# Performance work log

Hardware: AMD Instinct MI355X
Metric: run time of the kernel (lower is better)

Reference implementation:

```python
import jax, jax.numpy as jnp
import numpy as np

BETA = 0.05
KNN = 6
UL_ALPHA = 0.05
UL_BETA = 1.0


def setup_inputs() -> dict:
    key = jax.random.key(0)
    k1, k2, k3 = jax.random.split(key, 3)
    B, D, N = 256, 2048, 16384
    inputs = jax.random.normal(k1, (B, D), dtype=jnp.float32)
    em = jax.random.normal(k2, (N, D), dtype=jnp.float32)
    # exemplar memory rows are kept unit-norm by the update rule
    em = em / jnp.linalg.norm(em, axis=1, keepdims=True)
    targets = jax.random.randint(k3, (B,), 0, N, dtype=jnp.int64)
    return {"inputs": inputs, "em": em, "targets": targets, "epoch": 10}


def smooth_hot(logits, targets, em, k):
    # Vectorized k-reciprocal neighbor search (replaces the per-sample Python loop).
    m, n = logits.shape
    # index_sorted[:, :k] == top-k class indices per sample
    _, topk_idx = jax.lax.top_k(logits, k)            # [m, k]
    neigh = em[topk_idx]                               # [m, k, d]
    sims = jnp.einsum('mkd,nd->mkn', neigh, em)        # [m, k, n]
    _, neigh_topk = jax.lax.top_k(sims, k)             # [m, k, k]
    # neighbor j of sample i is reciprocal if anchor (top-1 of i) is in its top-k
    anchor = topk_idx[:, :1, None]                     # [m, 1, 1]
    recip = (neigh_topk == anchor).any(axis=-1)        # [m, k]
    weights = jnp.where(recip, 3.0 / k, 0.0).astype(logits.dtype)
    rows = jnp.arange(m)[:, None]
    onehot = jnp.zeros_like(logits).at[rows, topk_idx].set(weights)
    onehot = onehot.at[jnp.arange(m), targets].set(1.0)
    return onehot


def reference(inputs, em, targets, epoch):
    # ExemplarMemory.forward: similarity logits against the memory bank
    logits = (inputs @ em.T) / BETA                    # [B, N]
    # epoch >= 5 and knn > 0 branch (epoch=10)
    onehot = jax.lax.stop_gradient(
        smooth_hot(jax.lax.stop_gradient(logits), targets, em, KNN))
    logp = jax.nn.log_softmax(logits, axis=1)
    beta_loss = (-(onehot * logp).sum(axis=1)).mean()
    t_re = jnp.where(onehot == 0.0, jnp.float32(1e-4), onehot)
    alpha_loss = (-(jax.nn.softmax(logits, axis=1) * jnp.log(t_re)).sum(axis=1)).mean()
    return (UL_ALPHA * alpha_loss, UL_BETA * beta_loss)
```

## Files before the change

### kernel.cpp

```cpp
#include <hip/hip_runtime.h>
#include <math.h>

#define DIMK 2048
#define NEMB 16384
#define NB 256
#define NR2 1536
#define INV_BETA 20.0f
#define NEG_INF (-3.0e38f)

typedef short short8 __attribute__((ext_vector_type(8)));
typedef float f32x4 __attribute__((ext_vector_type(4)));

__device__ __forceinline__ unsigned short f2bf(float f) {
  unsigned u = __float_as_uint(f);
  u += 0x7fffu + ((u >> 16) & 1u);
  return (unsigned short)(u >> 16);
}

__device__ __forceinline__ void ins6i(float x, int xi, float v[6], int vi[6]) {
  if (x > v[5] || (x == v[5] && xi < vi[5])) {
    v[5] = x; vi[5] = xi;
#pragma unroll
    for (int j = 5; j > 0; j--) {
      if (v[j] > v[j - 1] || (v[j] == v[j - 1] && vi[j] < vi[j - 1])) {
        float tv = v[j]; v[j] = v[j - 1]; v[j - 1] = tv;
        int ti = vi[j]; vi[j] = vi[j - 1]; vi[j - 1] = ti;
      }
    }
  }
}

__global__ __launch_bounds__(256) void cvt_kernel(const float* __restrict__ src,
                                                  unsigned short* __restrict__ dst, int n4) {
  int i = blockIdx.x * 256 + threadIdx.x;
  if (i < n4) {
    float4 f = ((const float4*)src)[i];
    ushort4 o;
    o.x = f2bf(f.x); o.y = f2bf(f.y); o.z = f2bf(f.z); o.w = f2bf(f.w);
    ((ushort4*)dst)[i] = o;
  }
}

template <int MODE>
__global__ __launch_bounds__(256, 3) void gemm_rs(
    const unsigned short* __restrict__ Abase, const unsigned short* __restrict__ Bbase,
    const int* __restrict__ nidx, float* __restrict__ outP,
    const float* __restrict__ saIn, int* __restrict__ cntOut,
    const int* __restrict__ surv, const int* __restrict__ nsurvp) {
  constexpr int MTILE = (MODE == 0) ? 64 : 128;
  constexpr int MI = 4;
  constexpr int NI = (MODE == 0) ? 2 : 4;
  constexpr int NSUB_A = MTILE / 16;
  constexpr int NSUB = NSUB_A + 8;
  constexpr int NA = NSUB / 4;
  constexpr int NKC = (MODE == 1 || MODE == 2) ? 16 : 64;
  constexpr int OSTRIDE = (MODE == 0) ? 16384 : ((MODE == 1) ? 2048 : 14336);
  constexpr size_t PLANE =
      (MODE == 1) ? (size_t)1280 * 2048 : ((MODE == 2) ? (size_t)256 * 14336 : 0);

  __shared__ unsigned short st[2][NSUB * 512];
  __shared__ int rowIdxSh[128];
  __shared__ float saSh[128];
  __shared__ int cntSh[128];
  __shared__ int outRowSh[128];
  int t = threadIdx.x;
  int lane = t & 63, wave = t >> 6;
  int quad = lane >> 4, l16 = lane & 15;
  int wr = (MODE == 0) ? 0 : (wave >> 1);
  int wc = (MODE == 0) ? wave : (wave & 1);
  int bn = blockIdx.x, bm = blockIdx.y, kz = blockIdx.z;
  int nvalid = 128;

  if constexpr (MODE == 1) {
    if (t < 128) {
      int slot = bm * 128 + t;
      int g = (slot / 5) * 6 + (slot % 5) + 1;
      rowIdxSh[t] = nidx[g];
    }
    __syncthreads();
  }
  if constexpr (MODE == 2) {
    int ns = nsurvp[0];
    int nsCap = (ns < 256) ? ns : 256;
    if (bm * 128 >= nsCap) return;
    if (t < 128) {
      int idx = bm * 128 + t;
      rowIdxSh[t] = nidx[surv[(idx < nsCap) ? idx : 0]];
    }
    __syncthreads();
  }
  if constexpr (MODE == 3) {
    int ns = nsurvp[0];
    if (256 + bm * 128 >= ns) return;
    nvalid = ns - 256 - bm * 128;
    if (nvalid > 128) nvalid = 128;
    if (t < 128) {
      int idx = 256 + bm * 128 + ((t < nvalid) ? t : 0);
      int r = surv[idx];
      rowIdxSh[t] = nidx[r];
      saSh[t] = saIn[r];
      cntSh[t] = 0;
      outRowSh[t] = r;
    }
    __syncthreads();
  }

  int colbase = (MODE >= 2) ? ((bn + 16) * 128) : (bn * 128);
  int kbase = (MODE == 1 || MODE == 2) ? kz * (NKC * 32) : 0;

  const unsigned short* agp[NA];
  int soff[NA];
  {
    int seg = lane >> 4;
#pragma unroll
    for (int a = 0; a < NA; a++) {
      int s = wave + a * 4;
      size_t grow;
      const unsigned short* basep;
      if (s < NSUB_A) {
        int r = s * 16 + l16;
        grow = (MODE == 0) ? (size_t)(bm * MTILE + r) : (size_t)rowIdxSh[r];
        basep = Abase;
      } else {
        grow = (size_t)(colbase + (s - NSUB_A) * 16 + l16);
        basep = Bbase;
      }
      agp[a] = basep + grow * DIMK + kbase + seg * 8;
      soff[a] = s * 512;
    }
  }

  f32x4 acc[MI][NI];
#pragma unroll
  for (int mi = 0; mi < MI; mi++)
#pragma unroll
    for (int ni = 0; ni < NI; ni++) acc[mi][ni] = (f32x4)0.0f;

  int lo = lane * 8;

  short8 rA[NA], rB2[NA];
  auto LOADT = [&](short8* R, int kk) {
#pragma unroll
    for (int a = 0; a < NA; a++) R[a] = *(const short8*)(agp[a] + kk * 32);
  };
  auto WRITET = [&](const short8* R, int b) {
#pragma unroll
    for (int a = 0; a < NA; a++) *(short8*)&st[b][soff[a] + lo] = R[a];
  };
  auto COMPUTE = [&](int b) {
    const unsigned short* hb = &st[b][0];
    short8 af[MI], bfv[NI];
#pragma unroll
    for (int mi = 0; mi < MI; mi++)
      af[mi] = *(const short8*)&hb[(wr * MI + mi) * 512 + lo];
#pragma unroll
    for (int ni = 0; ni < NI; ni++)
      bfv[ni] = *(const short8*)&hb[(NSUB_A + wc * NI + ni) * 512 + lo];
#pragma unroll
    for (int mi = 0; mi < MI; mi++)
#pragma unroll
      for (int ni = 0; ni < NI; ni++)
        acc[mi][ni] =
            __builtin_amdgcn_mfma_f32_16x16x32_bf16(af[mi], bfv[ni], acc[mi][ni], 0, 0, 0);
  };

  LOADT(rA, 0);
  LOADT(rB2, 1);
  WRITET(rA, 0);
  __syncthreads();
  for (int k = 0; k < NKC; k += 2) {
    if (k + 2 < NKC) LOADT(rA, k + 2);
    COMPUTE(0);
    WRITET(rB2, 1);
    __syncthreads();
    if (k + 3 < NKC) LOADT(rB2, k + 3);
    COMPUTE(1);
    if (k + 2 < NKC) WRITET(rA, 0);
    __syncthreads();
  }

  if constexpr (MODE == 0) {
#pragma unroll
    for (int mi = 0; mi < MI; mi++) {
      int row = bm * MTILE + mi * 16 + quad * 4;
#pragma unroll
      for (int ni = 0; ni < NI; ni++) {
        int col = bn * 128 + wave * 32 + ni * 16 + l16;
#pragma unroll
        for (int rr = 0; rr < 4; rr++)
          outP[(size_t)(row + rr) * OSTRIDE + col] = acc[mi][ni][rr] * INV_BETA;
      }
    }
  } else if constexpr (MODE == 1 || MODE == 2) {
    float* op = outP + (size_t)kz * PLANE;
#pragma unroll
    for (int mi = 0; mi < MI; mi++) {
#pragma unroll
      for (int ni = 0; ni < NI; ni++) {
        int col = bn * 128 + wc * 64 + ni * 16 + l16;
#pragma unroll
        for (int rr = 0; rr < 4; rr++) {
          int row = bm * 128 + wr * 64 + mi * 16 + quad * 4 + rr;
          op[(size_t)row * OSTRIDE + col] = acc[mi][ni][rr];
        }
      }
    }
  } else {
#pragma unroll
    for (int mi = 0; mi < MI; mi++) {
#pragma unroll
      for (int rr = 0; rr < 4; rr++) {
        int rloc = wr * 64 + mi * 16 + quad * 4 + rr;
        float s = saSh[rloc];
        int c = 0;
#pragma unroll
        for (int ni = 0; ni < NI; ni++) c += (acc[mi][ni][rr] > s) ? 1 : 0;
        c += __shfl_xor(c, 1, 64);
        c += __shfl_xor(c, 2, 64);
        c += __shfl_xor(c, 4, 64);
        c += __shfl_xor(c, 8, 64);
        if (l16 == 0) atomicAdd(&cntSh[rloc], c);
      }
    }
    __syncthreads();
    if (t < nvalid) atomicAdd(&cntOut[outRowSh[t]], cntSh[t]);
  }
}

__global__ __launch_bounds__(256) void countA_kernel(const float* __restrict__ simsA,
                                                     const float* __restrict__ sa,
                                                     int* __restrict__ cnt) {
  int t = threadIdx.x, lane = t & 63;
  constexpr size_t PL = (size_t)1280 * 2048;
  for (int it = blockIdx.x; it < 1280 * 8; it += 256) {
    int slot = it >> 3, cx = it & 7;
    int g = (slot / 5) * 6 + (slot % 5) + 1;
    size_t o = (size_t)slot * 2048 + cx * 256 + t;
    float s = simsA[o] + simsA[o + PL] + simsA[o + 2 * PL] + simsA[o + 3 * PL];
    int c = (s > sa[g]) ? 1 : 0;
#pragma unroll
    for (int off = 32; off > 0; off >>= 1) c += __shfl_down(c, off, 64);
    if (lane == 0 && c > 0) atomicAdd(&cnt[g], c);
  }
}

__global__ __launch_bounds__(256) void countB_kernel(const float* __restrict__ simsB,
                                                     const float* __restrict__ sa,
                                                     const int* __restrict__ surv,
                                                     const int* __restrict__ nsurvp,
                                                     int* __restrict__ cnt) {
  int t = threadIdx.x, lane = t & 63;
  int ns = nsurvp[0];
  int nsCap = (ns < 256) ? ns : 256;
  constexpr size_t PL = (size_t)256 * 14336;
  int total = nsCap * 56;
  for (int it = blockIdx.x; it < total; it += 448) {
    int sv = it / 56, cx = it % 56;
    size_t o = (size_t)sv * 14336 + cx * 256 + t;
    float s = simsB[o] + simsB[o + PL] + simsB[o + 2 * PL] + simsB[o + 3 * PL];
    int w = surv[sv];
    int c = (s > sa[w]) ? 1 : 0;
#pragma unroll
    for (int off = 32; off > 0; off >>= 1) c += __shfl_down(c, off, 64);
    if (lane == 0 && c > 0) atomicAdd(&cnt[w], c);
  }
}

__global__ __launch_bounds__(256) void compact_kernel(const int* __restrict__ cnt,
                                                      int* __restrict__ surv,
                                                      int* __restrict__ nsurv) {
  __shared__ int ctr;
  if (threadIdx.x == 0) ctr = 0;
  __syncthreads();
  for (int i = threadIdx.x; i < NR2; i += 256) {
    if ((i % 6) != 0 && cnt[i] < 6) {
      int p = atomicAdd(&ctr, 1);
      surv[p] = i;
    }
  }
  __syncthreads();
  if (threadIdx.x == 0) nsurv[0] = ctr;
}

__global__ __launch_bounds__(1024) void rowstats_kernel(
    const float* __restrict__ logits, float* __restrict__ topv,
    int* __restrict__ topi, float* __restrict__ lse) {
  int m = blockIdx.x, t = threadIdx.x;
  const float4* row4 = (const float4*)(logits + (size_t)m * NEMB);
  float v6[6]; int i6[6];
#pragma unroll
  for (int j = 0; j < 6; j++) { v6[j] = NEG_INF; i6[j] = 0x7fffffff; }
  float vals[16];
#pragma unroll
  for (int j = 0; j < 4; j++) {
    float4 f = row4[t + j * 1024];
    vals[j * 4 + 0] = f.x; vals[j * 4 + 1] = f.y;
    vals[j * 4 + 2] = f.z; vals[j * 4 + 3] = f.w;
  }
  float mx = vals[0];
#pragma unroll
  for (int r = 1; r < 16; r++) mx = fmaxf(mx, vals[r]);
  float sme = 0.f;
#pragma unroll
  for (int r = 0; r < 16; r++) sme += expf(vals[r] - mx);
#pragma unroll
  for (int j = 0; j < 4; j++) {
    int base = (t + j * 1024) * 4;
#pragma unroll
    for (int b = 0; b < 4; b++) ins6i(vals[j * 4 + b], base + b, v6, i6);
  }
  __shared__ float sv[1024 * 6]; __shared__ int si[1024 * 6];
  __shared__ float smx[1024], ssm[1024];
#pragma unroll
  for (int j = 0; j < 6; j++) { sv[t * 6 + j] = v6[j]; si[t * 6 + j] = i6[j]; }
  smx[t] = mx; ssm[t] = sme;
  __syncthreads();
  for (int s = 512; s > 0; s >>= 1) {
    if (t < s) {
      float mo = smx[t + s], lo2 = ssm[t + s];
      float mn = fmaxf(smx[t], mo);
      ssm[t] = ssm[t] * expf(smx[t] - mn) + lo2 * expf(mo - mn);
      smx[t] = mn;
#pragma unroll
      for (int j = 0; j < 6; j++) ins6i(sv[(t + s) * 6 + j], si[(t + s) * 6 + j], v6, i6);
#pragma unroll
      for (int j = 0; j < 6; j++) { sv[t * 6 + j] = v6[j]; si[t * 6 + j] = i6[j]; }
    }
    __syncthreads();
  }
  if (t == 0) {
    lse[m] = smx[0] + logf(ssm[0]);
#pragma unroll
    for (int j = 0; j < 6; j++) { topv[m * 6 + j] = v6[j]; topi[m * 6 + j] = i6[j]; }
  }
}

__global__ __launch_bounds__(256) void sa_kernel(const float* __restrict__ em,
                                                 const int* __restrict__ topi,
                                                 float* __restrict__ sa,
                                                 int* __restrict__ cnt) {
  int gid = blockIdx.x * 256 + threadIdx.x;
  int w = gid >> 6, lane = gid & 63;
  if (w >= NR2) return;
  if (lane == 1) cnt[w] = 0;
  int m = w / 6;
  int i = topi[w], a = topi[m * 6];
  const float* ei = em + (size_t)i * DIMK;
  const float* ea = em + (size_t)a * DIMK;
  float s = 0.f;
  for (int d = lane; d < DIMK; d += 64) s += ei[d] * ea[d];
#pragma unroll
  for (int off = 32; off > 0; off >>= 1) s += __shfl_down(s, off, 64);
  if (lane == 0) sa[w] = s;
}

__global__ __launch_bounds__(256) void final_kernel(
    const float* __restrict__ logits, const float* __restrict__ topv,
    const int* __restrict__ topi, const float* __restrict__ lse_arr,
    const int* __restrict__ cnt, const int* __restrict__ targets,
    float* __restrict__ out) {
  int m = threadIdx.x;
  float lse = lse_arr[m];
  int tgt = targets[m];
  float tl = logits[(size_t)m * NEMB + tgt];
  float beta = 0.f, Ps = 0.f, nbp = 0.f;
  bool tin = false;
#pragma unroll
  for (int k = 0; k < 6; k++) {
    int idx = topi[m * 6 + k]; float v = topv[m * 6 + k];
    float p = expf(v - lse);
    if (idx == tgt) { tin = true; beta += (lse - v); Ps += p; }
    else if (cnt[m * 6 + k] < 6) { beta += 0.5f * (lse - v); Ps += p; nbp += p; }
  }
  if (!tin) { beta += (lse - tl); Ps += expf(tl - lse); }
  float alpha = 9.2103404f * (1.f - Ps) + 0.6931472f * nbp;
  __shared__ float sA[256], sB2[256];
  sA[m] = alpha; sB2[m] = beta;
  __syncthreads();
  for (int s = 128; s > 0; s >>= 1) {
    if (m < s) { sA[m] += sA[m + s]; sB2[m] += sB2[m + s]; }
    __syncthreads();
  }
  if (m == 0) { out[0] = 0.05f * sA[0] / 256.f; out[1] = sB2[0] / 256.f; }
}

extern "C" void kernel_launch(void* const* d_in, const int* in_sizes, int n_in,
                              void* d_out, int out_size, void* d_ws, size_t ws_size,
                              hipStream_t stream) {
  const float* x = (const float*)d_in[0];
  const float* em = (const float*)d_in[1];
  const int* targets = (const int*)d_in[2];
  char* ws = (char*)d_ws;
  unsigned short* em_bf = (unsigned short*)ws;
  unsigned short* x_bf  = (unsigned short*)(ws + 67108864);
  float* logits = (float*)(ws + 68157440);
  float* simsA  = (float*)(ws + 84934656);
  float* simsB  = (float*)(ws + 126877696);
  int*   cnt    = (int*)  (ws + 185597952);
  int*   surv   = (int*)  (ws + 185604096);
  int*   nsurv  = (int*)  (ws + 185610240);
  float* topv   = (float*)(ws + 185610304);
  int*   topi   = (int*)  (ws + 185616448);
  float* lse    = (float*)(ws + 185622592);
  float* sa     = (float*)(ws + 185623616);

  cvt_kernel<<<dim3(32768), dim3(256), 0, stream>>>(em, em_bf, NEMB * DIMK / 4);
  cvt_kernel<<<dim3(512), dim3(256), 0, stream>>>(x, x_bf, NB * DIMK / 4);
  gemm_rs<0><<<dim3(128, 4, 1), dim3(256), 0, stream>>>(
      x_bf, em_bf, (const int*)nullptr, logits, (const float*)nullptr, (int*)nullptr,
      (const int*)nullptr, (const int*)nullptr);
  rowstats_kernel<<<dim3(256), dim3(1024), 0, stream>>>(logits, topv, topi, lse);
  sa_kernel<<<dim3(384), dim3(256), 0, stream>>>(em, topi, sa, cnt);
  gemm_rs<1><<<dim3(16, 10, 4), dim3(256), 0, stream>>>(
      em_bf, em_bf, topi, simsA, (const float*)nullptr, (int*)nullptr,
      (const int*)nullptr, (const int*)nullptr);
  countA_kernel<<<dim3(256), dim3(256), 0, stream>>>(simsA, sa, cnt);
  compact_kernel<<<dim3(1), dim3(256), 0, stream>>>(cnt, surv, nsurv);
  gemm_rs<2><<<dim3(112, 2, 4), dim3(256), 0, stream>>>(
      em_bf, em_bf, topi, simsB, (const float*)nullptr, (int*)nullptr, surv, nsurv);
  countB_kernel<<<dim3(448), dim3(256), 0, stream>>>(simsB, sa, surv, nsurv, cnt);
  gemm_rs<3><<<dim3(112, 8, 1), dim3(256), 0, stream>>>(
      em_bf, em_bf, topi, (float*)nullptr, sa, cnt, surv, nsurv);
  final_kernel<<<dim3(1), dim3(256), 0, stream>>>(logits, topv, topi, lse, cnt, targets,
                                                  (float*)d_out);
}
```

Measured before the change: 414.7 us.

## Replace staged survivor GEMMs with prefilter-on-512-columns plus scalar pass over survivors

The reciprocal-neighbor count pipeline is restructured. The first split-K GEMM now covers only the first 512 memory columns with 16 K-splits. The surviving neighbor rows are then checked against the remaining columns by a new scalar dot-product kernel that reads bf16 rows from LDS. That kernel also compacts the survivors itself and performs the final loss reduction in the last block, using a done counter. Alongside this, the two conversion kernels are merged, the sa computation is folded into the rowstats kernel, and the MODE 2/3 GEMMs, compact and countB launches are removed. The scalar pass replaces matrix-core work with per-column shuffle reductions, which could be slow if many rows survive the prefilter.

```diff
diff --git a/kernel.cpp b/kernel.cpp
--- a/kernel.cpp
+++ b/kernel.cpp
@@ -7,6 +7,7 @@
 #define NR2 1536
 #define INV_BETA 20.0f
 #define NEG_INF (-3.0e38f)
+#define PBV_BLOCKS 124
 
 typedef short short8 __attribute__((ext_vector_type(8)));
 typedef float f32x4 __attribute__((ext_vector_type(4)));
@@ -16,6 +17,9 @@
   u += 0x7fffu + ((u >> 16) & 1u);
   return (unsigned short)(u >> 16);
 }
+__device__ __forceinline__ float bf2f(unsigned short u) {
+  return __uint_as_float(((unsigned)u) << 16);
+}
 
 __device__ __forceinline__ void ins6i(float x, int xi, float v[6], int vi[6]) {
   if (x > v[5] || (x == v[5] && xi < vi[5])) {
@@ -30,46 +34,44 @@
   }
 }
 
-__global__ __launch_bounds__(256) void cvt_kernel(const float* __restrict__ src,
-                                                  unsigned short* __restrict__ dst, int n4) {
-  int i = blockIdx.x * 256 + threadIdx.x;
-  if (i < n4) {
-    float4 f = ((const float4*)src)[i];
-    ushort4 o;
-    o.x = f2bf(f.x); o.y = f2bf(f.y); o.z = f2bf(f.z); o.w = f2bf(f.w);
-    ((ushort4*)dst)[i] = o;
-  }
+__global__ __launch_bounds__(256) void cvt2_kernel(const float* __restrict__ em,
+                                                   const float* __restrict__ x,
+                                                   unsigned short* __restrict__ em_bf,
+                                                   unsigned short* __restrict__ x_bf) {
+  int b = blockIdx.x, t = threadIdx.x;
+  const float* src;
+  unsigned short* dst;
+  int i;
+  if (b < 32768) { src = em; dst = em_bf; i = b * 256 + t; }
+  else           { src = x;  dst = x_bf;  i = (b - 32768) * 256 + t; }
+  float4 f = ((const float4*)src)[i];
+  ushort4 o;
+  o.x = f2bf(f.x); o.y = f2bf(f.y); o.z = f2bf(f.z); o.w = f2bf(f.w);
+  ((ushort4*)dst)[i] = o;
 }
 
 template <int MODE>
 __global__ __launch_bounds__(256, 3) void gemm_rs(
     const unsigned short* __restrict__ Abase, const unsigned short* __restrict__ Bbase,
-    const int* __restrict__ nidx, float* __restrict__ outP,
-    const float* __restrict__ saIn, int* __restrict__ cntOut,
-    const int* __restrict__ surv, const int* __restrict__ nsurvp) {
+    const int* __restrict__ nidx, float* __restrict__ outP) {
   constexpr int MTILE = (MODE == 0) ? 64 : 128;
   constexpr int MI = 4;
   constexpr int NI = (MODE == 0) ? 2 : 4;
   constexpr int NSUB_A = MTILE / 16;
   constexpr int NSUB = NSUB_A + 8;
   constexpr int NA = NSUB / 4;
-  constexpr int NKC = (MODE == 1 || MODE == 2) ? 16 : 64;
-  constexpr int OSTRIDE = (MODE == 0) ? 16384 : ((MODE == 1) ? 2048 : 14336);
-  constexpr size_t PLANE =
-      (MODE == 1) ? (size_t)1280 * 2048 : ((MODE == 2) ? (size_t)256 * 14336 : 0);
+  constexpr int NKC = (MODE == 1) ? 4 : 64;
+  constexpr int OSTRIDE = (MODE == 0) ? 16384 : 512;
+  constexpr size_t PLANE = (size_t)1280 * 512;
 
   __shared__ unsigned short st[2][NSUB * 512];
   __shared__ int rowIdxSh[128];
-  __shared__ float saSh[128];
-  __shared__ int cntSh[128];
-  __shared__ int outRowSh[128];
   int t = threadIdx.x;
   int lane = t & 63, wave = t >> 6;
   int quad = lane >> 4, l16 = lane & 15;
   int wr = (MODE == 0) ? 0 : (wave >> 1);
   int wc = (MODE == 0) ? wave : (wave & 1);
   int bn = blockIdx.x, bm = blockIdx.y, kz = blockIdx.z;
-  int nvalid = 128;
 
   if constexpr (MODE == 1) {
     if (t < 128) {
@@ -79,34 +81,8 @@
     }
     __syncthreads();
   }
-  if constexpr (MODE == 2) {
-    int ns = nsurvp[0];
-    int nsCap = (ns < 256) ? ns : 256;
-    if (bm * 128 >= nsCap) return;
-    if (t < 128) {
-      int idx = bm * 128 + t;
-      rowIdxSh[t] = nidx[surv[(idx < nsCap) ? idx : 0]];
-    }
-    __syncthreads();
-  }
-  if constexpr (MODE == 3) {
-    int ns = nsurvp[0];
-    if (256 + bm * 128 >= ns) return;
-    nvalid = ns - 256 - bm * 128;
-    if (nvalid > 128) nvalid = 128;
-    if (t < 128) {
-      int idx = 256 + bm * 128 + ((t < nvalid) ? t : 0);
-      int r = surv[idx];
-      rowIdxSh[t] = nidx[r];
-      saSh[t] = saIn[r];
-      cntSh[t] = 0;
-      outRowSh[t] = r;
-    }
-    __syncthreads();
-  }
-
-  int colbase = (MODE >= 2) ? ((bn + 16) * 128) : (bn * 128);
-  int kbase = (MODE == 1 || MODE == 2) ? kz * (NKC * 32) : 0;
+
+  int kbase = (MODE == 1) ? kz * (NKC * 32) : 0;
 
   const unsigned short* agp[NA];
   int soff[NA];
@@ -122,7 +98,7 @@
         grow = (MODE == 0) ? (size_t)(bm * MTILE + r) : (size_t)rowIdxSh[r];
         basep = Abase;
       } else {
-        grow = (size_t)(colbase + (s - NSUB_A) * 16 + l16);
+        grow = (size_t)(bn * 128 + (s - NSUB_A) * 16 + l16);
         basep = Bbase;
       }
       agp[a] = basep + grow * DIMK + kbase + seg * 8;
@@ -191,7 +167,7 @@
           outP[(size_t)(row + rr) * OSTRIDE + col] = acc[mi][ni][rr] * INV_BETA;
       }
     }
-  } else if constexpr (MODE == 1 || MODE == 2) {
+  } else {
     float* op = outP + (size_t)kz * PLANE;
 #pragma unroll
     for (int mi = 0; mi < MI; mi++) {
@@ -205,25 +181,6 @@
         }
       }
     }
-  } else {
-#pragma unroll
-    for (int mi = 0; mi < MI; mi++) {
-#pragma unroll
-      for (int rr = 0; rr < 4; rr++) {
-        int rloc = wr * 64 + mi * 16 + quad * 4 + rr;
-        float s = saSh[rloc];
-        int c = 0;
-#pragma unroll
-        for (int ni = 0; ni < NI; ni++) c += (acc[mi][ni][rr] > s) ? 1 : 0;
-        c += __shfl_xor(c, 1, 64);
-        c += __shfl_xor(c, 2, 64);
-        c += __shfl_xor(c, 4, 64);
-        c += __shfl_xor(c, 8, 64);
-        if (l16 == 0) atomicAdd(&cntSh[rloc], c);
-      }
-    }
-    __syncthreads();
-    if (t < nvalid) atomicAdd(&cntOut[outRowSh[t]], cntSh[t]);
   }
 }
 
@@ -231,12 +188,14 @@
                                                      const float* __restrict__ sa,
                                                      int* __restrict__ cnt) {
   int t = threadIdx.x, lane = t & 63;
-  constexpr size_t PL = (size_t)1280 * 2048;
-  for (int it = blockIdx.x; it < 1280 * 8; it += 256) {
-    int slot = it >> 3, cx = it & 7;
+  constexpr size_t PL = (size_t)1280 * 512;
+  for (int it = blockIdx.x; it < 1280 * 2; it += 256) {
+    int slot = it >> 1, cx = it & 1;
     int g = (slot / 5) * 6 + (slot % 5) + 1;
-    size_t o = (size_t)slot * 2048 + cx * 256 + t;
-    float s = simsA[o] + simsA[o + PL] + simsA[o + 2 * PL] + simsA[o + 3 * PL];
+    size_t o = (size_t)slot * 512 + cx * 256 + t;
+    float s = 0.f;
+#pragma unroll
+    for (int p = 0; p < 16; p++) s += simsA[o + (size_t)p * PL];
     int c = (s > sa[g]) ? 1 : 0;
 #pragma unroll
     for (int off = 32; off > 0; off >>= 1) c += __shfl_down(c, off, 64);
@@ -244,48 +203,12 @@
   }
 }
 
-__global__ __launch_bounds__(256) void countB_kernel(const float* __restrict__ simsB,
-                                                     const float* __restrict__ sa,
-                                                     const int* __restrict__ surv,
-                                                     const int* __restrict__ nsurvp,
-                                                     int* __restrict__ cnt) {
-  int t = threadIdx.x, lane = t & 63;
-  int ns = nsurvp[0];
-  int nsCap = (ns < 256) ? ns : 256;
-  constexpr size_t PL = (size_t)256 * 14336;
-  int total = nsCap * 56;
-  for (int it = blockIdx.x; it < total; it += 448) {
-    int sv = it / 56, cx = it % 56;
-    size_t o = (size_t)sv * 14336 + cx * 256 + t;
-    float s = simsB[o] + simsB[o + PL] + simsB[o + 2 * PL] + simsB[o + 3 * PL];
-    int w = surv[sv];
-    int c = (s > sa[w]) ? 1 : 0;
-#pragma unroll
-    for (int off = 32; off > 0; off >>= 1) c += __shfl_down(c, off, 64);
-    if (lane == 0 && c > 0) atomicAdd(&cnt[w], c);
-  }
-}
-
-__global__ __launch_bounds__(256) void compact_kernel(const int* __restrict__ cnt,
-                                                      int* __restrict__ surv,
-                                                      int* __restrict__ nsurv) {
-  __shared__ int ctr;
-  if (threadIdx.x == 0) ctr = 0;
-  __syncthreads();
-  for (int i = threadIdx.x; i < NR2; i += 256) {
-    if ((i % 6) != 0 && cnt[i] < 6) {
-      int p = atomicAdd(&ctr, 1);
-      surv[p] = i;
-    }
-  }
-  __syncthreads();
-  if (threadIdx.x == 0) nsurv[0] = ctr;
-}
-
-__global__ __launch_bounds__(1024) void rowstats_kernel(
-    const float* __restrict__ logits, float* __restrict__ topv,
-    int* __restrict__ topi, float* __restrict__ lse) {
+__global__ __launch_bounds__(1024) void rowstats_sa_kernel(
+    const float* __restrict__ logits, const float* __restrict__ em,
+    float* __restrict__ topv, int* __restrict__ topi, float* __restrict__ lse,
+    float* __restrict__ sa, int* __restrict__ cnt, int* __restrict__ done) {
   int m = blockIdx.x, t = threadIdx.x;
+  int lane = t & 63, wave = t >> 6;
   const float4* row4 = (const float4*)(logits + (size_t)m * NEMB);
   float v6[6]; int i6[6];
 #pragma unroll
@@ -332,56 +255,114 @@
     lse[m] = smx[0] + logf(ssm[0]);
 #pragma unroll
     for (int j = 0; j < 6; j++) { topv[m * 6 + j] = v6[j]; topi[m * 6 + j] = i6[j]; }
-  }
-}
-
-__global__ __launch_bounds__(256) void sa_kernel(const float* __restrict__ em,
-                                                 const int* __restrict__ topi,
-                                                 float* __restrict__ sa,
-                                                 int* __restrict__ cnt) {
-  int gid = blockIdx.x * 256 + threadIdx.x;
-  int w = gid >> 6, lane = gid & 63;
-  if (w >= NR2) return;
-  if (lane == 1) cnt[w] = 0;
-  int m = w / 6;
-  int i = topi[w], a = topi[m * 6];
-  const float* ei = em + (size_t)i * DIMK;
-  const float* ea = em + (size_t)a * DIMK;
-  float s = 0.f;
-  for (int d = lane; d < DIMK; d += 64) s += ei[d] * ea[d];
-#pragma unroll
-  for (int off = 32; off > 0; off >>= 1) s += __shfl_down(s, off, 64);
-  if (lane == 0) sa[w] = s;
-}
-
-__global__ __launch_bounds__(256) void final_kernel(
+    if (m == 0) done[0] = 0;
+  }
+  if (wave < 6) {
+    int ii = si[wave], aa = si[0];
+    const float* ei = em + (size_t)ii * DIMK;
+    const float* ea = em + (size_t)aa * DIMK;
+    float s = 0.f;
+    for (int d = lane; d < DIMK; d += 64) s += ei[d] * ea[d];
+#pragma unroll
+    for (int off = 32; off > 0; off >>= 1) s += __shfl_down(s, off, 64);
+    if (lane == 0) { sa[m * 6 + wave] = s; cnt[m * 6 + wave] = 0; }
+  }
+}
+
+__global__ __launch_bounds__(256) void pbv_kernel(
+    const unsigned short* __restrict__ em_bf, const int* __restrict__ topi,
+    const float* __restrict__ sa, int* __restrict__ cnt, int* __restrict__ done,
     const float* __restrict__ logits, const float* __restrict__ topv,
-    const int* __restrict__ topi, const float* __restrict__ lse_arr,
-    const int* __restrict__ cnt, const int* __restrict__ targets,
+    const float* __restrict__ lse_arr, const int* __restrict__ targets,
     float* __restrict__ out) {
-  int m = threadIdx.x;
-  float lse = lse_arr[m];
-  int tgt = targets[m];
-  float tl = logits[(size_t)m * NEMB + tgt];
-  float beta = 0.f, Ps = 0.f, nbp = 0.f;
-  bool tin = false;
-#pragma unroll
-  for (int k = 0; k < 6; k++) {
-    int idx = topi[m * 6 + k]; float v = topv[m * 6 + k];
-    float p = expf(v - lse);
-    if (idx == tgt) { tin = true; beta += (lse - v); Ps += p; }
-    else if (cnt[m * 6 + k] < 6) { beta += 0.5f * (lse - v); Ps += p; nbp += p; }
-  }
-  if (!tin) { beta += (lse - tl); Ps += expf(tl - lse); }
-  float alpha = 9.2103404f * (1.f - Ps) + 0.6931472f * nbp;
+  __shared__ int survSh[1536];
+  __shared__ int nsSh;
+  __shared__ unsigned short rowsSh[16][2048];
+  __shared__ int ldsCnt[16];
+  __shared__ int lastFlag;
   __shared__ float sA[256], sB2[256];
-  sA[m] = alpha; sB2[m] = beta;
-  __syncthreads();
-  for (int s = 128; s > 0; s >>= 1) {
-    if (m < s) { sA[m] += sA[m + s]; sB2[m] += sB2[m + s]; }
-    __syncthreads();
-  }
-  if (m == 0) { out[0] = 0.05f * sA[0] / 256.f; out[1] = sB2[0] / 256.f; }
+  int t = threadIdx.x, lane = t & 63, wave = t >> 6;
+  if (t == 0) nsSh = 0;
+  __syncthreads();
+  for (int i = t; i < NR2; i += 256) {
+    if ((i % 6) != 0 && cnt[i] < 6) {
+      int p = atomicAdd(&nsSh, 1);
+      survSh[p] = i;
+    }
+  }
+  __syncthreads();
+  int ns = nsSh;
+  int colbase = 512 + blockIdx.x * 128;
+
+  for (int g = 0; g < ns; g += 16) {
+    int gsz = (ns - g < 16) ? (ns - g) : 16;
+    for (int ri = 0; ri < gsz; ri++) {
+      int r = topi[survSh[g + ri]];
+      ((short8*)&rowsSh[ri][0])[t] = ((const short8*)(em_bf + (size_t)r * DIMK))[t];
+    }
+    if (t < 16) ldsCnt[t] = 0;
+    __syncthreads();
+    for (int j = 0; j < 32; j++) {
+      int col = colbase + wave * 32 + j;
+      const short8* cp = (const short8*)(em_bf + (size_t)col * DIMK + lane * 32);
+      short8 c0 = cp[0], c1 = cp[1], c2 = cp[2], c3 = cp[3];
+      float cf[32];
+#pragma unroll
+      for (int e = 0; e < 8; e++) {
+        cf[e] = bf2f((unsigned short)c0[e]);
+        cf[8 + e] = bf2f((unsigned short)c1[e]);
+        cf[16 + e] = bf2f((unsigned short)c2[e]);
+        cf[24 + e] = bf2f((unsigned short)c3[e]);
+      }
+      for (int ri = 0; ri < gsz; ri++) {
+        const unsigned short* rp = &rowsSh[ri][lane * 32];
+        float s = 0.f;
+#pragma unroll
+        for (int e = 0; e < 32; e++) s += cf[e] * bf2f(rp[e]);
+#pragma unroll
+        for (int off = 32; off > 0; off >>= 1) s += __shfl_down(s, off, 64);
+        if (lane == 0 && s > sa[survSh[g + ri]]) atomicAdd(&ldsCnt[ri], 1);
+      }
+    }
+    __syncthreads();
+    if (t < gsz) {
+      if (ldsCnt[t] > 0) atomicAdd(&cnt[survSh[g + t]], ldsCnt[t]);
+    }
+    __syncthreads();
+  }
+
+  __threadfence();
+  if (t == 0) {
+    int old = atomicAdd(done, 1);
+    lastFlag = (old == PBV_BLOCKS - 1) ? 1 : 0;
+  }
+  __syncthreads();
+  if (!lastFlag) return;
+  __threadfence();
+  {
+    int m = t;
+    float lse = lse_arr[m];
+    int tgt = targets[m];
+    float tl = logits[(size_t)m * NEMB + tgt];
+    float beta = 0.f, Ps = 0.f, nbp = 0.f;
+    bool tin = false;
+#pragma unroll
+    for (int k = 0; k < 6; k++) {
+      int idx = topi[m * 6 + k]; float v = topv[m * 6 + k];
+      float p = expf(v - lse);
+      if (idx == tgt) { tin = true; beta += (lse - v); Ps += p; }
+      else if (cnt[m * 6 + k] < 6) { beta += 0.5f * (lse - v); Ps += p; nbp += p; }
+    }
+    if (!tin) { beta += (lse - tl); Ps += expf(tl - lse); }
+    float alpha = 9.2103404f * (1.f - Ps) + 0.6931472f * nbp;
+    sA[m] = alpha; sB2[m] = beta;
+    __syncthreads();
+    for (int s = 128; s > 0; s >>= 1) {
+      if (m < s) { sA[m] += sA[m + s]; sB2[m] += sB2[m + s]; }
+      __syncthreads();
+    }
+    if (m == 0) { out[0] = 0.05f * sA[0] / 256.f; out[1] = sB2[0] / 256.f; }
+  }
 }
 
 extern "C" void kernel_launch(void* const* d_in, const int* in_sizes, int n_in,
@@ -395,32 +376,21 @@
   unsigned short* x_bf  = (unsigned short*)(ws + 67108864);
   float* logits = (float*)(ws + 68157440);
   float* simsA  = (float*)(ws + 84934656);
-  float* simsB  = (float*)(ws + 126877696);
-  int*   cnt    = (int*)  (ws + 185597952);
-  int*   surv   = (int*)  (ws + 185604096);
-  int*   nsurv  = (int*)  (ws + 185610240);
-  float* topv   = (float*)(ws + 185610304);
-  int*   topi   = (int*)  (ws + 185616448);
-  float* lse    = (float*)(ws + 185622592);
-  float* sa     = (float*)(ws + 185623616);
-
-  cvt_kernel<<<dim3(32768), dim3(256), 0, stream>>>(em, em_bf, NEMB * DIMK / 4);
-  cvt_kernel<<<dim3(512), dim3(256), 0, stream>>>(x, x_bf, NB * DIMK / 4);
-  gemm_rs<0><<<dim3(128, 4, 1), dim3(256), 0, stream>>>(
-      x_bf, em_bf, (const int*)nullptr, logits, (const float*)nullptr, (int*)nullptr,
-      (const int*)nullptr, (const int*)nullptr);
-  rowstats_kernel<<<dim3(256), dim3(1024), 0, stream>>>(logits, topv, topi, lse);
-  sa_kernel<<<dim3(384), dim3(256), 0, stream>>>(em, topi, sa, cnt);
-  gemm_rs<1><<<dim3(16, 10, 4), dim3(256), 0, stream>>>(
-      em_bf, em_bf, topi, simsA, (const float*)nullptr, (int*)nullptr,
-      (const int*)nullptr, (const int*)nullptr);
+  int*   cnt    = (int*)  (ws + 126877696);
+  float* topv   = (float*)(ws + 126883840);
+  int*   topi   = (int*)  (ws + 126889984);
+  float* lse    = (float*)(ws + 126896128);
+  float* sa     = (float*)(ws + 126897152);
+  int*   done   = (int*)  (ws + 126903296);
+
+  cvt2_kernel<<<dim3(33280), dim3(256), 0, stream>>>(em, x, em_bf, x_bf);
+  gemm_rs<0><<<dim3(128, 4, 1), dim3(256), 0, stream>>>(x_bf, em_bf, (const int*)nullptr,
+                                                        logits);
+  rowstats_sa_kernel<<<dim3(256), dim3(1024), 0, stream>>>(logits, em, topv, topi, lse,
+                                                           sa, cnt, done);
+  gemm_rs<1><<<dim3(4, 10, 16), dim3(256), 0, stream>>>(em_bf, em_bf, topi, simsA);
   countA_kernel<<<dim3(256), dim3(256), 0, stream>>>(simsA, sa, cnt);
-  compact_kernel<<<dim3(1), dim3(256), 0, stream>>>(cnt, surv, nsurv);
-  gemm_rs<2><<<dim3(112, 2, 4), dim3(256), 0, stream>>>(
-      em_bf, em_bf, topi, simsB, (const float*)nullptr, (int*)nullptr, surv, nsurv);
-  countB_kernel<<<dim3(448), dim3(256), 0, stream>>>(simsB, sa, surv, nsurv, cnt);
-  gemm_rs<3><<<dim3(112, 8, 1), dim3(256), 0, stream>>>(
-      em_bf, em_bf, topi, (float*)nullptr, sa, cnt, surv, nsurv);
-  final_kernel<<<dim3(1), dim3(256), 0, stream>>>(logits, topv, topi, lse, cnt, targets,
-                                                  (float*)d_out);
-}
+  pbv_kernel<<<dim3(PBV_BLOCKS), dim3(256), 0, stream>>>(em_bf, topi, sa, cnt, done,
+                                                         logits, topv, lse, targets,
+                                                         (float*)d_out);
+}
```

Measured after the change: 791.0 us. +90.7%, slower.
